# Kernel optimization log

Hardware: AMD Instinct MI355X
Metric: run time of the kernel (lower is better)

## Reference

```python
import jax, jax.numpy as jnp
import numpy as np

B, C, H, W, D = 2, 256, 40, 40, 40
HEADS = 8


def _conv1x1(x, w, b):
    # 1x1x1 Conv3d == pointwise channel mix: x [B,C,H,W,D], w [O,C], b [O]
    return jnp.einsum('bchwd,oc->bohwd', x, w) + b[None, :, None, None, None]


def setup_inputs() -> dict:
    key = jax.random.key(0)
    ks = jax.random.split(key, 9)
    s = 1.0 / np.sqrt(C)
    return {
        'x': jax.random.normal(ks[0], (B, C, H, W, D), dtype=jnp.float32),
        'wq': jax.random.normal(ks[1], (C, C), dtype=jnp.float32) * s,
        'bq': jax.random.normal(ks[2], (C,), dtype=jnp.float32) * 0.01,
        'wk': jax.random.normal(ks[3], (C, C), dtype=jnp.float32) * s,
        'bk': jax.random.normal(ks[4], (C,), dtype=jnp.float32) * 0.01,
        'wv': jax.random.normal(ks[5], (C, C), dtype=jnp.float32) * s,
        'bv': jax.random.normal(ks[6], (C,), dtype=jnp.float32) * 0.01,
        'wp': jax.random.normal(ks[7], (C, C), dtype=jnp.float32) * s,
        'bp': jax.random.normal(ks[8], (C,), dtype=jnp.float32) * 0.01,
    }


def reference(x, wq, bq, wk, bk, wv, bv, wp, bp):
    b, ch, h, w, d = x.shape
    heads = HEADS
    hd = ch // heads
    scale = hd ** -0.5
    # q/k/v projections are identical across the three branches -> compute once
    q = _conv1x1(x, wq, bq)
    k = _conv1x1(x, wk, bk)
    v = _conv1x1(x, wv, bv)

    def branch(s1, s2, s3):
        # row-major reshape, exactly matching torch .view semantics
        qh = q.reshape(b, heads, hd, s1, s2, s3)
        kh = k.reshape(b, heads, hd, s1, s2, s3)
        vh = v.reshape(b, heads, hd, s1, s2, s3)
        # matmul over last two axes: attend along s2 with s3 as feature dim
        attn = jax.nn.softmax(qh @ jnp.swapaxes(kh, -1, -2) * scale, axis=-1)
        return (attn @ vh).reshape(b, ch, h, w, d)

    out = branch(h, w, d) + branch(w, h, d) + branch(d, h, w)
    return _conv1x1(out, wp, bp)
```

## Files before the change

### kernel.cpp

```cpp
#include <hip/hip_runtime.h>

#define NB 2
#define NC 256
#define NHH 40
#define NSP 64000
#define PL 1600
#define SCALE 0.17677669529663687f

typedef unsigned short u16;
typedef unsigned int   u32;

typedef __attribute__((ext_vector_type(8))) short bf16x8;
typedef __attribute__((ext_vector_type(4))) float f32x4;

__device__ __forceinline__ float bf2f(u16 u) {
    union { u32 i; float f; } c; c.i = ((u32)u) << 16; return c.f;
}
__device__ __forceinline__ u16 f2bf(float f) {
    union { u32 i; float f; } c; c.f = f; u32 x = c.i;
    return (u16)((x + 0x7fffu + ((x >> 16) & 1u)) >> 16);
}
__device__ __forceinline__ u32 pack2(float a, float b) {
    return (u32)f2bf(a) | ((u32)f2bf(b) << 16);
}
__device__ __forceinline__ f32x4 zero4() {
    f32x4 z; z[0] = 0.f; z[1] = 0.f; z[2] = 0.f; z[3] = 0.f; return z;
}
__device__ __forceinline__ bf16x8 zero8() {
    bf16x8 z;
#pragma unroll
    for (int e = 0; e < 8; ++e) z[e] = 0;
    return z;
}

__global__ __launch_bounds__(256) void wcvt3(
    const float* __restrict__ wq, const float* __restrict__ wk,
    const float* __restrict__ wv, u16* __restrict__ dst)
{
    const int g   = blockIdx.x * 256 + threadIdx.x;
    const int mat = g >> 14;
    const int off = (g & 16383) << 2;
    const float* s = (mat == 0) ? wq : ((mat == 1) ? wk : wv);
    const float4 f = *(const float4*)(s + off);
    ushort4 p;
    p.x = f2bf(f.x); p.y = f2bf(f.y); p.z = f2bf(f.z); p.w = f2bf(f.w);
    *(ushort4*)(dst + (mat << 16) + off) = p;
}

__global__ __launch_bounds__(256) void wcvt1(
    const float* __restrict__ w, u16* __restrict__ dst)
{
    const int g   = blockIdx.x * 256 + threadIdx.x;
    const int off = g << 2;
    const float4 f = *(const float4*)(w + off);
    ushort4 p;
    p.x = f2bf(f.x); p.y = f2bf(f.y); p.z = f2bf(f.z); p.w = f2bf(f.w);
    *(ushort4*)(dst + off) = p;
}

__global__ __launch_bounds__(512, 4) void qkv4(
    const float* __restrict__ x, const u16* __restrict__ wb,
    const float* __restrict__ bq, const float* __restrict__ bk,
    const float* __restrict__ bv,
    u16* __restrict__ q, u16* __restrict__ k, u16* __restrict__ v)
{
    const int b    = blockIdx.z;
    const int n0   = blockIdx.x * 64;
    const int t    = threadIdx.x;
    const int lane = t & 63;
    const int wid  = t >> 6;
    const int o0w  = wid * 32;
    const int row  = lane & 15;
    const int kg   = (lane >> 4) << 3;
    const int g4   = (lane >> 4) << 2;

    __shared__ u16 xs[64][264];
    __shared__ u16 wsm[2][256][40];

    const float* xb = x + (size_t)b * NC * NSP;

    {
        const int p   = t >> 4;
        const int nn  = (t & 15) << 2;
        const int rot = (t >> 1) & 3;
#pragma unroll
        for (int it = 0; it < 4; ++it) {
            const int c = (it * 32 + p) * 2;
            const float4 fa = *(const float4*)(xb + (size_t)c * NSP + n0 + nn);
            const float4 fb = *(const float4*)(xb + (size_t)(c + 1) * NSP + n0 + nn);
            u32 pk[4] = { pack2(fa.x, fb.x), pack2(fa.y, fb.y),
                          pack2(fa.z, fb.z), pack2(fa.w, fb.w) };
#pragma unroll
            for (int kk = 0; kk < 4; ++kk) {
                const int k2 = (kk + rot) & 3;
                *(u32*)&xs[nn + k2][c] = pk[k2];
            }
        }
    }

    const int wrow = t >> 1;
    const int wseg = (t & 1) << 4;
    {
        const u16* ws0 = wb + (size_t)wrow * NC + wseg;
        *(bf16x8*)&wsm[0][wrow][wseg]     = *(const bf16x8*)(ws0);
        *(bf16x8*)&wsm[0][wrow][wseg + 8] = *(const bf16x8*)(ws0 + 8);
    }
    __syncthreads();

    f32x4 acc[2][4];
#pragma unroll
    for (int i = 0; i < 2; ++i)
#pragma unroll
        for (int j = 0; j < 4; ++j) acc[i][j] = zero4();

    int cur = 0;
    for (int step = 0; step < 24; ++step) {
        const int m  = step >> 3;
        const int kc = step & 7;
        const bool pf = (step + 1 < 24);

        bf16x8 wreg[2];
        if (pf) {
            const int m2  = (step + 1) >> 3;
            const int kc2 = (step + 1) & 7;
            const u16* ws2 = wb + ((size_t)m2 << 16) + (size_t)wrow * NC
                                + kc2 * 32 + wseg;
            wreg[0] = *(const bf16x8*)(ws2);
            wreg[1] = *(const bf16x8*)(ws2 + 8);
        }

        bf16x8 af[2], bfr[4];
#pragma unroll
        for (int i = 0; i < 2; ++i)
            af[i] = *(const bf16x8*)&wsm[cur][o0w + 16 * i + row][kg];
#pragma unroll
        for (int j = 0; j < 4; ++j)
            bfr[j] = *(const bf16x8*)&xs[16 * j + row][kc * 32 + kg];
#pragma unroll
        for (int i = 0; i < 2; ++i)
#pragma unroll
            for (int j = 0; j < 4; ++j)
                acc[i][j] = __builtin_amdgcn_mfma_f32_16x16x32_bf16(
                    af[i], bfr[j], acc[i][j], 0, 0, 0);

        if (pf) {
            *(bf16x8*)&wsm[cur ^ 1][wrow][wseg]     = wreg[0];
            *(bf16x8*)&wsm[cur ^ 1][wrow][wseg + 8] = wreg[1];
        }

        if (kc == 7) {
            u16* op = ((m == 0) ? q : ((m == 1) ? k : v)) + (size_t)b * NC * NSP;
            const float* bm = (m == 0) ? bq : ((m == 1) ? bk : bv);
#pragma unroll
            for (int i = 0; i < 2; ++i) {
#pragma unroll
                for (int r = 0; r < 4; ++r) {
                    const int o = o0w + 16 * i + g4 + r;
                    const float bb = bm[o];
#pragma unroll
                    for (int j = 0; j < 4; ++j) {
                        const int n = n0 + 16 * j + row;
                        op[(size_t)o * NSP + n] = f2bf(acc[i][j][r] + bb);
                    }
                }
            }
#pragma unroll
            for (int i = 0; i < 2; ++i)
#pragma unroll
                for (int j = 0; j < 4; ++j) acc[i][j] = zero4();
        }

        if (pf) {
            __syncthreads();
            cur ^= 1;
        }
    }
}

__global__ __launch_bounds__(64, 4) void attn_mfma(
    const u16* __restrict__ q, const u16* __restrict__ k,
    const u16* __restrict__ v, u16* __restrict__ a)
{
    const int s = blockIdx.x;
    const size_t base = (size_t)s * PL;
    const int l = threadIdx.x & 63;
    const int g = l >> 4;
    const int c = l & 15;

    __shared__ u16 vs[48][56];
    __shared__ u16 ps[48][56];

#pragma unroll
    for (int it = 0; it < 3; ++it) {
        const int t = l + it * 64;
        *(u32*)&vs[t >> 2][40 + ((t & 3) << 1)] = 0u;
    }

#pragma unroll
    for (int it = 0; it < 7; ++it) {
        const int idx = l + it * 64;
        if (idx < 400) {
            const int j = idx / 10, d4 = (idx % 10) << 2;
            const ushort4 vv = *(const ushort4*)(v + base + j * 40 + d4);
            vs[d4 + 0][j] = vv.x; vs[d4 + 1][j] = vv.y;
            vs[d4 + 2][j] = vv.z; vs[d4 + 3][j] = vv.w;
        }
    }

    f32x4 sacc[3][3];
#pragma unroll
    for (int mt = 0; mt < 3; ++mt)
#pragma unroll
        for (int jt = 0; jt < 3; ++jt) sacc[mt][jt] = zero4();

    {
        bf16x8 aq[3], bk0[3];
#pragma unroll
        for (int mt = 0; mt < 3; ++mt)
            aq[mt] = *(const bf16x8*)(q + base + (size_t)(mt * 16 + c) * 40 + g * 8);
#pragma unroll
        for (int jt = 0; jt < 3; ++jt)
            bk0[jt] = *(const bf16x8*)(k + base + (size_t)(jt * 16 + c) * 40 + g * 8);
#pragma unroll
        for (int mt = 0; mt < 3; ++mt)
#pragma unroll
            for (int jt = 0; jt < 3; ++jt)
                sacc[mt][jt] = __builtin_amdgcn_mfma_f32_16x16x32_bf16(
                    aq[mt], bk0[jt], sacc[mt][jt], 0, 0, 0);

        bf16x8 aq1[3], bk1[3];
#pragma unroll
        for (int mt = 0; mt < 3; ++mt)
            aq1[mt] = (g == 0)
                ? *(const bf16x8*)(q + base + (size_t)(mt * 16 + c) * 40 + 32)
                : zero8();
#pragma unroll
        for (int jt = 0; jt < 3; ++jt)
            bk1[jt] = (g == 0)
                ? *(const bf16x8*)(k + base + (size_t)(jt * 16 + c) * 40 + 32)
                : zero8();
#pragma unroll
        for (int mt = 0; mt < 3; ++mt)
#pragma unroll
            for (int jt = 0; jt < 3; ++jt)
                sacc[mt][jt] = __builtin_amdgcn_mfma_f32_16x16x32_bf16(
                    aq1[mt], bk1[jt], sacc[mt][jt], 0, 0, 0);
    }

    const bool val2 = (c < 8);
#pragma unroll
    for (int mt = 0; mt < 3; ++mt) {
#pragma unroll
        for (int r = 0; r < 4; ++r) {
            const float v0 = sacc[mt][0][r];
            const float v1 = sacc[mt][1][r];
            const float v2 = sacc[mt][2][r];
            float mx = fmaxf(fmaxf(v0, v1), val2 ? v2 : -1e30f);
#pragma unroll
            for (int off = 1; off < 16; off <<= 1)
                mx = fmaxf(mx, __shfl_xor(mx, off, 64));
            const float p0 = __expf((v0 - mx) * SCALE);
            const float p1 = __expf((v1 - mx) * SCALE);
            const float p2 = val2 ? __expf((v2 - mx) * SCALE) : 0.f;
            float sum = p0 + p1 + p2;
#pragma unroll
            for (int off = 1; off < 16; off <<= 1)
                sum += __shfl_xor(sum, off, 64);
            const float inv = 3.0f / sum;
            const int ri = mt * 16 + g * 4 + r;
            ps[ri][c]      = f2bf(p0 * inv);
            ps[ri][c + 16] = f2bf(p1 * inv);
            ps[ri][c + 32] = f2bf(p2 * inv);
        }
    }
    __syncthreads();

    f32x4 oacc[3][3];
#pragma unroll
    for (int mt = 0; mt < 3; ++mt)
#pragma unroll
        for (int nt = 0; nt < 3; ++nt) oacc[mt][nt] = zero4();

    {
        bf16x8 pa[3], vb_[3];
#pragma unroll
        for (int mt = 0; mt < 3; ++mt)
            pa[mt] = *(const bf16x8*)&ps[mt * 16 + c][g * 8];
#pragma unroll
        for (int nt = 0; nt < 3; ++nt)
            vb_[nt] = *(const bf16x8*)&vs[nt * 16 + c][g * 8];
#pragma unroll
        for (int mt = 0; mt < 3; ++mt)
#pragma unroll
            for (int nt = 0; nt < 3; ++nt)
                oacc[mt][nt] = __builtin_amdgcn_mfma_f32_16x16x32_bf16(
                    pa[mt], vb_[nt], oacc[mt][nt], 0, 0, 0);

        bf16x8 pa1[3], vb1[3];
#pragma unroll
        for (int mt = 0; mt < 3; ++mt)
            pa1[mt] = (g < 2) ? *(const bf16x8*)&ps[mt * 16 + c][32 + g * 8] : zero8();
#pragma unroll
        for (int nt = 0; nt < 3; ++nt)
            vb1[nt] = (g < 2) ? *(const bf16x8*)&vs[nt * 16 + c][32 + g * 8] : zero8();
#pragma unroll
        for (int mt = 0; mt < 3; ++mt)
#pragma unroll
            for (int nt = 0; nt < 3; ++nt)
                oacc[mt][nt] = __builtin_amdgcn_mfma_f32_16x16x32_bf16(
                    pa1[mt], vb1[nt], oacc[mt][nt], 0, 0, 0);
    }
    __syncthreads();

#pragma unroll
    for (int mt = 0; mt < 3; ++mt) {
        if (mt == 2 && g >= 2) continue;
#pragma unroll
        for (int r = 0; r < 4; ++r) {
            const int ri = mt * 16 + g * 4 + r;
#pragma unroll
            for (int nt = 0; nt < 3; ++nt) {
                if (nt == 2 && c >= 8) continue;
                ps[ri][nt * 16 + c] = f2bf(oacc[mt][nt][r]);
            }
        }
    }
    __syncthreads();

#pragma unroll
    for (int it = 0; it < 7; ++it) {
        const int idx = l + it * 64;
        if (idx < 400) {
            const int i = idx / 10, d4 = (idx % 10) << 2;
            *(ushort4*)(a + base + (size_t)idx * 4) = *(const ushort4*)&ps[i][d4];
        }
    }
}

__global__ __launch_bounds__(512, 4) void proj4(
    const u16* __restrict__ a, const u16* __restrict__ wpb,
    const float* __restrict__ bp, float* __restrict__ out)
{
    const int b    = blockIdx.z;
    const int n0   = blockIdx.x * 64;
    const int t    = threadIdx.x;
    const int lane = t & 63;
    const int wid  = t >> 6;
    const int o0w  = wid * 32;
    const int row  = lane & 15;
    const int kg   = (lane >> 4) << 3;
    const int g4   = (lane >> 4) << 2;

    __shared__ u16 xs[64][264];
    __shared__ u16 wsm[2][256][40];

    const u16* ab = a + (size_t)b * NC * NSP;

    {
        const int p   = t >> 4;
        const int nn  = (t & 15) << 2;
        const int rot = (t >> 1) & 3;
#pragma unroll
        for (int it = 0; it < 4; ++it) {
            const int c = (it * 32 + p) * 2;
            const ushort4 ua = *(const ushort4*)(ab + (size_t)c * NSP + n0 + nn);
            const ushort4 ub = *(const ushort4*)(ab + (size_t)(c + 1) * NSP + n0 + nn);
            u32 pk[4] = { (u32)ua.x | ((u32)ub.x << 16), (u32)ua.y | ((u32)ub.y << 16),
                          (u32)ua.z | ((u32)ub.z << 16), (u32)ua.w | ((u32)ub.w << 16) };
#pragma unroll
            for (int kk = 0; kk < 4; ++kk) {
                const int k2 = (kk + rot) & 3;
                *(u32*)&xs[nn + k2][c] = pk[k2];
            }
        }
    }

    const int wrow = t >> 1;
    const int wseg = (t & 1) << 4;
    {
        const u16* ws0 = wpb + (size_t)wrow * NC + wseg;
        *(bf16x8*)&wsm[0][wrow][wseg]     = *(const bf16x8*)(ws0);
        *(bf16x8*)&wsm[0][wrow][wseg + 8] = *(const bf16x8*)(ws0 + 8);
    }
    __syncthreads();

    f32x4 acc[2][4];
#pragma unroll
    for (int i = 0; i < 2; ++i)
#pragma unroll
        for (int j = 0; j < 4; ++j) acc[i][j] = zero4();

    int cur = 0;
    for (int step = 0; step < 8; ++step) {
        const bool pf = (step + 1 < 8);
        bf16x8 wreg[2];
        if (pf) {
            const u16* ws2 = wpb + (size_t)wrow * NC + (step + 1) * 32 + wseg;
            wreg[0] = *(const bf16x8*)(ws2);
            wreg[1] = *(const bf16x8*)(ws2 + 8);
        }

        bf16x8 af[2], bfr[4];
#pragma unroll
        for (int i = 0; i < 2; ++i)
            af[i] = *(const bf16x8*)&wsm[cur][o0w + 16 * i + row][kg];
#pragma unroll
        for (int j = 0; j < 4; ++j)
            bfr[j] = *(const bf16x8*)&xs[16 * j + row][step * 32 + kg];
#pragma unroll
        for (int i = 0; i < 2; ++i)
#pragma unroll
            for (int j = 0; j < 4; ++j)
                acc[i][j] = __builtin_amdgcn_mfma_f32_16x16x32_bf16(
                    af[i], bfr[j], acc[i][j], 0, 0, 0);

        if (pf) {
            *(bf16x8*)&wsm[cur ^ 1][wrow][wseg]     = wreg[0];
            *(bf16x8*)&wsm[cur ^ 1][wrow][wseg + 8] = wreg[1];
            __syncthreads();
            cur ^= 1;
        }
    }

    float* ob = out + (size_t)b * NC * NSP;
#pragma unroll
    for (int i = 0; i < 2; ++i) {
#pragma unroll
        for (int r = 0; r < 4; ++r) {
            const int o = o0w + 16 * i + g4 + r;
            const float bb = bp[o];
#pragma unroll
            for (int j = 0; j < 4; ++j) {
                const int n = n0 + 16 * j + row;
                ob[(size_t)o * NSP + n] = acc[i][j][r] + bb;
            }
        }
    }
}

extern "C" void kernel_launch(void* const* d_in, const int* in_sizes, int n_in,
                              void* d_out, int out_size, void* d_ws, size_t ws_size,
                              hipStream_t stream)
{
    const float* x  = (const float*)d_in[0];
    const float* wq = (const float*)d_in[1];
    const float* bq = (const float*)d_in[2];
    const float* wk = (const float*)d_in[3];
    const float* bk = (const float*)d_in[4];
    const float* wv = (const float*)d_in[5];
    const float* bv = (const float*)d_in[6];
    const float* wp = (const float*)d_in[7];
    const float* bp = (const float*)d_in[8];
    float* out = (float*)d_out;

    const size_t QE = (size_t)NB * NC * NSP;
    u16* qb = (u16*)d_ws;
    u16* kb = qb + QE;
    u16* vb = kb + QE;
    u16* ab = vb + QE;

    u16* wqkv = (u16*)d_out;
    u16* wpb  = qb;

    wcvt3<<<192, 256, 0, stream>>>(wq, wk, wv, wqkv);
    qkv4<<<dim3(NSP / 64, 1, NB), 512, 0, stream>>>(
        x, wqkv, bq, bk, bv, qb, kb, vb);
    attn_mfma<<<dim3(NB * NC * NHH), 64, 0, stream>>>(qb, kb, vb, ab);
    wcvt1<<<64, 256, 0, stream>>>(wp, wpb);
    proj4<<<dim3(NSP / 64, 1, NB), 512, 0, stream>>>(ab, wpb, bp, out);
}
```

Baseline: 249.0 us.

## Pre-swizzle weights into MFMA fragment order and load directly to registers

Weight conversion kernels now write bf16 weights in per-wave MFMA A-fragment order, so the QKV and projection GEMMs load A fragments straight from global memory into registers with a one-step prefetch. The double-buffered shared-memory weight tile and its per-step __syncthreads are removed, which cuts LDS use (possibly raising occupancy) and barrier stalls. In exchange, every wave issues its own global/L2 weight loads each step and relies on cache hits.

```diff
diff --git a/kernel.cpp b/kernel.cpp
--- a/kernel.cpp
+++ b/kernel.cpp
@@ -33,33 +33,53 @@
     return z;
 }
 
-__global__ __launch_bounds__(256) void wcvt3(
+__global__ __launch_bounds__(256) void wfrag3(
     const float* __restrict__ wq, const float* __restrict__ wk,
     const float* __restrict__ wv, u16* __restrict__ dst)
 {
-    const int g   = blockIdx.x * 256 + threadIdx.x;
-    const int mat = g >> 14;
-    const int off = (g & 16383) << 2;
-    const float* s = (mat == 0) ? wq : ((mat == 1) ? wk : wv);
-    const float4 f = *(const float4*)(s + off);
-    ushort4 p;
-    p.x = f2bf(f.x); p.y = f2bf(f.y); p.z = f2bf(f.z); p.w = f2bf(f.w);
-    *(ushort4*)(dst + (mat << 16) + off) = p;
-}
-
-__global__ __launch_bounds__(256) void wcvt1(
+    const int gid  = blockIdx.x * 256 + threadIdx.x;
+    const int lane = gid & 63;
+    const int i    = (gid >> 6) & 1;
+    const int wid  = (gid >> 7) & 7;
+    const int step = gid >> 10;
+    const int m    = step >> 3;
+    const int kc   = step & 7;
+    const int row  = wid * 32 + i * 16 + (lane & 15);
+    const int col  = kc * 32 + ((lane >> 4) << 3);
+    const float* s = ((m == 0) ? wq : ((m == 1) ? wk : wv)) + (size_t)row * NC + col;
+    const float4 a = *(const float4*)(s);
+    const float4 b = *(const float4*)(s + 4);
+    ushort4 p0, p1;
+    p0.x = f2bf(a.x); p0.y = f2bf(a.y); p0.z = f2bf(a.z); p0.w = f2bf(a.w);
+    p1.x = f2bf(b.x); p1.y = f2bf(b.y); p1.z = f2bf(b.z); p1.w = f2bf(b.w);
+    u16* d = dst + (size_t)gid * 8;
+    *(ushort4*)(d)     = p0;
+    *(ushort4*)(d + 4) = p1;
+}
+
+__global__ __launch_bounds__(256) void wfrag1(
     const float* __restrict__ w, u16* __restrict__ dst)
 {
-    const int g   = blockIdx.x * 256 + threadIdx.x;
-    const int off = g << 2;
-    const float4 f = *(const float4*)(w + off);
-    ushort4 p;
-    p.x = f2bf(f.x); p.y = f2bf(f.y); p.z = f2bf(f.z); p.w = f2bf(f.w);
-    *(ushort4*)(dst + off) = p;
-}
-
-__global__ __launch_bounds__(512, 4) void qkv4(
-    const float* __restrict__ x, const u16* __restrict__ wb,
+    const int gid  = blockIdx.x * 256 + threadIdx.x;
+    const int lane = gid & 63;
+    const int i    = (gid >> 6) & 1;
+    const int wid  = (gid >> 7) & 7;
+    const int step = (gid >> 10) & 7;
+    const int row  = wid * 32 + i * 16 + (lane & 15);
+    const int col  = step * 32 + ((lane >> 4) << 3);
+    const float* s = w + (size_t)row * NC + col;
+    const float4 a = *(const float4*)(s);
+    const float4 b = *(const float4*)(s + 4);
+    ushort4 p0, p1;
+    p0.x = f2bf(a.x); p0.y = f2bf(a.y); p0.z = f2bf(a.z); p0.w = f2bf(a.w);
+    p1.x = f2bf(b.x); p1.y = f2bf(b.y); p1.z = f2bf(b.z); p1.w = f2bf(b.w);
+    u16* d = dst + (size_t)gid * 8;
+    *(ushort4*)(d)     = p0;
+    *(ushort4*)(d + 4) = p1;
+}
+
+__global__ __launch_bounds__(512, 4) void qkv5(
+    const float* __restrict__ x, const u16* __restrict__ wf,
     const float* __restrict__ bq, const float* __restrict__ bk,
     const float* __restrict__ bv,
     u16* __restrict__ q, u16* __restrict__ k, u16* __restrict__ v)
@@ -75,7 +95,6 @@
     const int g4   = (lane >> 4) << 2;
 
     __shared__ u16 xs[64][264];
-    __shared__ u16 wsm[2][256][40];
 
     const float* xb = x + (size_t)b * NC * NSP;
 
@@ -97,42 +116,32 @@
             }
         }
     }
-
-    const int wrow = t >> 1;
-    const int wseg = (t & 1) << 4;
-    {
-        const u16* ws0 = wb + (size_t)wrow * NC + wseg;
-        *(bf16x8*)&wsm[0][wrow][wseg]     = *(const bf16x8*)(ws0);
-        *(bf16x8*)&wsm[0][wrow][wseg + 8] = *(const bf16x8*)(ws0 + 8);
-    }
     __syncthreads();
 
+    const u16* wfb = wf + (size_t)(wid * 2) * 512 + (size_t)lane * 8;
+
     f32x4 acc[2][4];
 #pragma unroll
     for (int i = 0; i < 2; ++i)
 #pragma unroll
         for (int j = 0; j < 4; ++j) acc[i][j] = zero4();
 
-    int cur = 0;
+    bf16x8 afc[2], afn[2];
+    afc[0] = *(const bf16x8*)(wfb);
+    afc[1] = *(const bf16x8*)(wfb + 512);
+
     for (int step = 0; step < 24; ++step) {
         const int m  = step >> 3;
         const int kc = step & 7;
         const bool pf = (step + 1 < 24);
 
-        bf16x8 wreg[2];
         if (pf) {
-            const int m2  = (step + 1) >> 3;
-            const int kc2 = (step + 1) & 7;
-            const u16* ws2 = wb + ((size_t)m2 << 16) + (size_t)wrow * NC
-                                + kc2 * 32 + wseg;
-            wreg[0] = *(const bf16x8*)(ws2);
-            wreg[1] = *(const bf16x8*)(ws2 + 8);
-        }
-
-        bf16x8 af[2], bfr[4];
-#pragma unroll
-        for (int i = 0; i < 2; ++i)
-            af[i] = *(const bf16x8*)&wsm[cur][o0w + 16 * i + row][kg];
+            const u16* wn = wfb + (size_t)(step + 1) * 8192;
+            afn[0] = *(const bf16x8*)(wn);
+            afn[1] = *(const bf16x8*)(wn + 512);
+        }
+
+        bf16x8 bfr[4];
 #pragma unroll
         for (int j = 0; j < 4; ++j)
             bfr[j] = *(const bf16x8*)&xs[16 * j + row][kc * 32 + kg];
@@ -141,12 +150,7 @@
 #pragma unroll
             for (int j = 0; j < 4; ++j)
                 acc[i][j] = __builtin_amdgcn_mfma_f32_16x16x32_bf16(
-                    af[i], bfr[j], acc[i][j], 0, 0, 0);
-
-        if (pf) {
-            *(bf16x8*)&wsm[cur ^ 1][wrow][wseg]     = wreg[0];
-            *(bf16x8*)&wsm[cur ^ 1][wrow][wseg + 8] = wreg[1];
-        }
+                    afc[i], bfr[j], acc[i][j], 0, 0, 0);
 
         if (kc == 7) {
             u16* op = ((m == 0) ? q : ((m == 1) ? k : v)) + (size_t)b * NC * NSP;
@@ -170,10 +174,8 @@
                 for (int j = 0; j < 4; ++j) acc[i][j] = zero4();
         }
 
-        if (pf) {
-            __syncthreads();
-            cur ^= 1;
-        }
+        afc[0] = afn[0];
+        afc[1] = afn[1];
     }
 }
 
@@ -337,8 +339,8 @@
     }
 }
 
-__global__ __launch_bounds__(512, 4) void proj4(
-    const u16* __restrict__ a, const u16* __restrict__ wpb,
+__global__ __launch_bounds__(512, 4) void proj5(
+    const u16* __restrict__ a, const u16* __restrict__ wf,
     const float* __restrict__ bp, float* __restrict__ out)
 {
     const int b    = blockIdx.z;
@@ -352,7 +354,6 @@
     const int g4   = (lane >> 4) << 2;
 
     __shared__ u16 xs[64][264];
-    __shared__ u16 wsm[2][256][40];
 
     const u16* ab = a + (size_t)b * NC * NSP;
 
@@ -374,36 +375,30 @@
             }
         }
     }
-
-    const int wrow = t >> 1;
-    const int wseg = (t & 1) << 4;
-    {
-        const u16* ws0 = wpb + (size_t)wrow * NC + wseg;
-        *(bf16x8*)&wsm[0][wrow][wseg]     = *(const bf16x8*)(ws0);
-        *(bf16x8*)&wsm[0][wrow][wseg + 8] = *(const bf16x8*)(ws0 + 8);
-    }
     __syncthreads();
 
+    const u16* wfb = wf + (size_t)(wid * 2) * 512 + (size_t)lane * 8;
+
     f32x4 acc[2][4];
 #pragma unroll
     for (int i = 0; i < 2; ++i)
 #pragma unroll
         for (int j = 0; j < 4; ++j) acc[i][j] = zero4();
 
-    int cur = 0;
+    bf16x8 afc[2], afn[2];
+    afc[0] = *(const bf16x8*)(wfb);
+    afc[1] = *(const bf16x8*)(wfb + 512);
+
+#pragma unroll
     for (int step = 0; step < 8; ++step) {
         const bool pf = (step + 1 < 8);
-        bf16x8 wreg[2];
         if (pf) {
-            const u16* ws2 = wpb + (size_t)wrow * NC + (step + 1) * 32 + wseg;
-            wreg[0] = *(const bf16x8*)(ws2);
-            wreg[1] = *(const bf16x8*)(ws2 + 8);
-        }
-
-        bf16x8 af[2], bfr[4];
-#pragma unroll
-        for (int i = 0; i < 2; ++i)
-            af[i] = *(const bf16x8*)&wsm[cur][o0w + 16 * i + row][kg];
+            const u16* wn = wfb + (size_t)(step + 1) * 8192;
+            afn[0] = *(const bf16x8*)(wn);
+            afn[1] = *(const bf16x8*)(wn + 512);
+        }
+
+        bf16x8 bfr[4];
 #pragma unroll
         for (int j = 0; j < 4; ++j)
             bfr[j] = *(const bf16x8*)&xs[16 * j + row][step * 32 + kg];
@@ -412,14 +407,10 @@
 #pragma unroll
             for (int j = 0; j < 4; ++j)
                 acc[i][j] = __builtin_amdgcn_mfma_f32_16x16x32_bf16(
-                    af[i], bfr[j], acc[i][j], 0, 0, 0);
-
-        if (pf) {
-            *(bf16x8*)&wsm[cur ^ 1][wrow][wseg]     = wreg[0];
-            *(bf16x8*)&wsm[cur ^ 1][wrow][wseg + 8] = wreg[1];
-            __syncthreads();
-            cur ^= 1;
-        }
+                    afc[i], bfr[j], acc[i][j], 0, 0, 0);
+
+        afc[0] = afn[0];
+        afc[1] = afn[1];
     }
 
     float* ob = out + (size_t)b * NC * NSP;
@@ -459,13 +450,13 @@
     u16* vb = kb + QE;
     u16* ab = vb + QE;
 
-    u16* wqkv = (u16*)d_out;
-    u16* wpb  = qb;
-
-    wcvt3<<<192, 256, 0, stream>>>(wq, wk, wv, wqkv);
-    qkv4<<<dim3(NSP / 64, 1, NB), 512, 0, stream>>>(
-        x, wqkv, bq, bk, bv, qb, kb, vb);
+    u16* wqf = (u16*)d_out;
+    u16* wpf = qb;
+
+    wfrag3<<<96, 256, 0, stream>>>(wq, wk, wv, wqf);
+    qkv5<<<dim3(NSP / 64, 1, NB), 512, 0, stream>>>(
+        x, wqf, bq, bk, bv, qb, kb, vb);
     attn_mfma<<<dim3(NB * NC * NHH), 64, 0, stream>>>(qb, kb, vb, ab);
-    wcvt1<<<64, 256, 0, stream>>>(wp, wpb);
-    proj4<<<dim3(NSP / 64, 1, NB), 512, 0, stream>>>(ab, wpb, bp, out);
-}
+    wfrag1<<<32, 256, 0, stream>>>(wp, wpf);
+    proj5<<<dim3(NSP / 64, 1, NB), 512, 0, stream>>>(ab, wpf, bp, out);
+}
```

Result: faster. 235.0 us (median of 2 runs) (-5.6%).
